# Kernel tuning notes

Hardware: AMD Instinct MI355X
Metric: run time of the kernel (lower is better)

Reference implementation:

```python
import jax, jax.numpy as jnp
import numpy as np

D = 192          # d_model = d_perc = d_tech
H = 3            # n_heads
HD = D // H      # head_dim = 64
FP = 128         # fingerprint_dim
EPS_LN = 1e-5


def _layernorm(x, g, b):
    mu = jnp.mean(x, axis=-1, keepdims=True)
    var = jnp.var(x, axis=-1, keepdims=True)
    return (x - mu) * jax.lax.rsqrt(var + EPS_LN) * g + b


def setup_inputs() -> dict:
    key = jax.random.key(0)
    ks = jax.random.split(key, 32)
    B = 65536
    s = 0.05
    inp = {
        'perc_vec': jax.random.normal(ks[0], (B, D), jnp.float32),
        'tech_vec': jax.random.normal(ks[1], (B, D), jnp.float32),
        # proj_p / proj_t (torch Linear: [out, in])
        'Wp': jax.random.normal(ks[2], (D, D), jnp.float32) * s,
        'bp': jax.random.normal(ks[3], (D,), jnp.float32) * s,
        'Wt': jax.random.normal(ks[4], (D, D), jnp.float32) * s,
        'bt': jax.random.normal(ks[5], (D,), jnp.float32) * s,
        # MultiheadAttention packed in-proj [3D, D] and out-proj [D, D]
        'in_w': jax.random.normal(ks[6], (3 * D, D), jnp.float32) * s,
        'in_b': jax.random.normal(ks[7], (3 * D,), jnp.float32) * s,
        'out_w': jax.random.normal(ks[8], (D, D), jnp.float32) * s,
        'out_b': jax.random.normal(ks[9], (D,), jnp.float32) * s,
        # FFN
        'ffn_w1': jax.random.normal(ks[10], (2 * D, D), jnp.float32) * s,
        'ffn_b1': jax.random.normal(ks[11], (2 * D,), jnp.float32) * s,
        'ffn_w2': jax.random.normal(ks[12], (D, 2 * D), jnp.float32) * s,
        'ffn_b2': jax.random.normal(ks[13], (D,), jnp.float32) * s,
        # LayerNorms
        'ln1_g': jnp.ones((D,), jnp.float32),
        'ln1_b': jnp.zeros((D,), jnp.float32),
        'ln2_g': jnp.ones((D,), jnp.float32),
        'ln2_b': jnp.zeros((D,), jnp.float32),
        # classifier head
        'cls_w1': jax.random.normal(ks[14], (D, D), jnp.float32) * s,
        'cls_b1': jax.random.normal(ks[15], (D,), jnp.float32) * s,
        'cls_w2': jax.random.normal(ks[16], (3, D), jnp.float32) * s,
        'cls_b2': jax.random.normal(ks[17], (3,), jnp.float32) * s,
        # fingerprint head
        'fp_w': jax.random.normal(ks[18], (FP, D), jnp.float32) * s,
        'fp_b': jax.random.normal(ks[19], (FP,), jnp.float32) * s,
    }
    return inp


def reference(perc_vec, tech_vec, Wp, bp, Wt, bt, in_w, in_b, out_w, out_b,
              ffn_w1, ffn_b1, ffn_w2, ffn_b2, ln1_g, ln1_b, ln2_g, ln2_b,
              cls_w1, cls_b1, cls_w2, cls_b2, fp_w, fp_b):
    B = perc_vec.shape[0]
    # projections -> 2-token sequence [B, 2, D]
    p = perc_vec @ Wp.T + bp
    t = tech_vec @ Wt.T + bt
    seq = jnp.stack([p, t], axis=1)

    # self-attention (eval mode, no dropout)
    qkv = seq @ in_w.T + in_b                     # [B, 2, 3D]
    q, k, v = jnp.split(qkv, 3, axis=-1)
    q = q.reshape(B, 2, H, HD).transpose(0, 2, 1, 3)  # [B, H, 2, HD]
    k = k.reshape(B, 2, H, HD).transpose(0, 2, 1, 3)
    v = v.reshape(B, 2, H, HD).transpose(0, 2, 1, 3)
    scores = jnp.einsum('bhqd,bhkd->bhqk', q, k) / np.sqrt(HD).astype(np.float32)
    attn = jax.nn.softmax(scores, axis=-1)
    ctx = jnp.einsum('bhqk,bhkd->bhqd', attn, v)      # [B, H, 2, HD]
    ctx = ctx.transpose(0, 2, 1, 3).reshape(B, 2, D)
    attn_out = ctx @ out_w.T + out_b

    x = _layernorm(seq + attn_out, ln1_g, ln1_b)
    h = jax.nn.relu(x @ ffn_w1.T + ffn_b1)
    ffn = h @ ffn_w2.T + ffn_b2
    x = _layernorm(x + ffn, ln2_g, ln2_b)

    z = x.mean(axis=1)                                # [B, D]
    logits = jax.nn.relu(z @ cls_w1.T + cls_b1) @ cls_w2.T + cls_b2  # [B, 3]
    probs = jax.nn.sigmoid(logits)
    fp = z @ fp_w.T + fp_b
    fp = fp / jnp.maximum(jnp.linalg.norm(fp, axis=-1, keepdims=True), 1e-12)
    # (presence_p, decode_reliability, artifact_risk, fingerprint)
    return probs[:, 0:1], probs[:, 1:2], probs[:, 2:3], fp
```

## Files before the change

kernel.cpp:

```cpp
#include <hip/hip_runtime.h>
#include <hip/hip_bf16.h>
#include <math.h>

#define D 192
#define RPB 16
typedef unsigned short u16;
typedef __attribute__((ext_vector_type(8))) short short8;
typedef __attribute__((ext_vector_type(4))) float float4v;

__device__ __forceinline__ float b2f(u16 u){ union{unsigned i; float f;}c; c.i=(unsigned)u<<16; return c.f; }
__device__ __forceinline__ u16  f2b(float f){
    union{float f; unsigned i;}c; c.f=f;
    unsigned r = c.i + 0x7FFFu + ((c.i>>16)&1u);
    return (u16)(r>>16);
}
__device__ __forceinline__ float sel4(float a0,float a1,float a2,float a3,int s){
    return s==0?a0:(s==1?a1:(s==2?a2:a3));
}

#define WP_OFF   0
#define WT_OFF   36864
#define INW_OFF  73728
#define OUTW_OFF 184320
#define FW1_OFF  221184
#define FW2_OFF  294912
#define CW1_OFF  368640
#define FPW_OFF  405504
#define W_TOTAL  430080

__global__ __launch_bounds__(256)
void cvt_weights(const float* __restrict__ Wp, const float* __restrict__ Wt,
                 const float* __restrict__ in_w, const float* __restrict__ out_w,
                 const float* __restrict__ fw1, const float* __restrict__ fw2,
                 const float* __restrict__ cw1, const float* __restrict__ fpw,
                 u16* __restrict__ ws)
{
    int idx = blockIdx.x * 256 + threadIdx.x;
    if (idx >= W_TOTAL) return;
    const float* src; int off; int K = 192;
    if      (idx < WT_OFF)   { src = Wp;   off = WP_OFF; }
    else if (idx < INW_OFF)  { src = Wt;   off = WT_OFF; }
    else if (idx < OUTW_OFF) { src = in_w; off = INW_OFF; }
    else if (idx < FW1_OFF)  { src = out_w;off = OUTW_OFF; }
    else if (idx < FW2_OFF)  { src = fw1;  off = FW1_OFF; }
    else if (idx < CW1_OFF)  { src = fw2;  off = FW2_OFF; K = 384; }
    else if (idx < FPW_OFF)  { src = cw1;  off = CW1_OFF; }
    else                     { src = fpw;  off = FPW_OFF; }
    int lin = idx - off;
    int n = lin / K, k = lin - n*K;
    int swz = ((n>>4)*(K>>5) + (k>>5))*512 + ((n&15)<<5) + (k&31);
    ws[off + swz] = f2b(src[lin]);
}

template<int KT, int MT>
__device__ __forceinline__ void load_afrags(short8 (&A)[MT][KT], const u16* base,
                                            int stride, int lane16, int quad)
{
    #pragma unroll
    for (int mt = 0; mt < MT; ++mt)
        #pragma unroll
        for (int ks = 0; ks < KT; ++ks)
            A[mt][ks] = *(const short8*)(base + (mt*16 + lane16)*stride + ks*32 + quad*8);
}

template<int KT, int MT, int NTW>
__device__ __forceinline__ void run_gemm(const short8 (&A)[MT][KT],
    const u16* __restrict__ wsb, const float* __restrict__ bias,
    u16* dst, float* dstf, int dstride,
    const u16* resid, int rstride, bool relu, int rmul, int roff,
    int wave, int lane16, int quad)
{
    #pragma unroll
    for (int i = 0; i < NTW; ++i) {
        int nt = wave + 4*i, n0 = nt*16;
        float4v c[MT];
        #pragma unroll
        for (int mt = 0; mt < MT; ++mt) c[mt] = (float4v){0.f,0.f,0.f,0.f};
        #pragma unroll
        for (int ks = 0; ks < KT; ++ks) {
            short8 b = *(const short8*)(wsb + (size_t)((nt*KT + ks)<<9) + (lane16<<5) + (quad<<3));
            #pragma unroll
            for (int mt = 0; mt < MT; ++mt)
                c[mt] = __builtin_amdgcn_mfma_f32_16x16x32_bf16(A[mt][ks], b, c[mt], 0,0,0);
        }
        float bv = bias[n0 + lane16];
        #pragma unroll
        for (int mt = 0; mt < MT; ++mt)
            #pragma unroll
            for (int ii = 0; ii < 4; ++ii) {
                int dr = (mt*16 + quad*4 + ii)*rmul + roff;
                float v = c[mt][ii] + bv;
                if (resid) v += b2f(resid[dr*rstride + n0 + lane16]);
                if (relu)  v = fmaxf(v, 0.f);
                if (dst) dst [dr*dstride + n0 + lane16] = f2b(v);
                else     dstf[dr*dstride + n0 + lane16] = v;
            }
    }
}

#define S1 200
#define SH 392
#define A_STG_P 0
#define A_STG_T 3200
#define A_SEQ 12544
#define A_CTX 0
#define A_X1  12544
#define A_H   0
#define A_Z   0
#define A_CH  3200
#define A_FPF 6400
#define ARENA_U16 18944

__global__ __launch_bounds__(256, 3)
void fusion_mfma_kernel(
    const float* __restrict__ perc, const float* __restrict__ tech,
    const float* __restrict__ bp,   const float* __restrict__ bt,
    const float* __restrict__ in_b, const float* __restrict__ out_b,
    const float* __restrict__ fb1,  const float* __restrict__ fb2,
    const float* __restrict__ ln1g, const float* __restrict__ ln1b,
    const float* __restrict__ ln2g, const float* __restrict__ ln2b,
    const float* __restrict__ cb1,  const float* __restrict__ cw2,
    const float* __restrict__ cb2,  const float* __restrict__ fpb,
    const u16*   __restrict__ ws,
    float* __restrict__ out, int B)
{
    __shared__ __align__(16) u16 arena[ARENA_U16];
    __shared__ __align__(16) float satt[16][3][4];
    __shared__ float wavered[4][32][2];
    __shared__ float srn[16];

    const int tid = threadIdx.x;
    const int wave = tid >> 6, lane = tid & 63;
    const int lane16 = lane & 15, quad = lane >> 4;
    const int row0 = blockIdx.x * RPB;
    float* fpf = (float*)(arena + A_FPF);

    #pragma unroll
    for (int it = 0; it < 3; ++it) {
        int idx = it*256 + tid;
        int arr = idx >= 384 ? 1 : 0;
        int rem = arr ? idx - 384 : idx;
        int r = rem / 24, g = rem - r*24;
        const float* src = arr ? tech : perc;
        const float4* s4 = (const float4*)(src + (size_t)(row0 + r)*D + g*8);
        float4 lo = s4[0], hi = s4[1];
        short8 o;
        o[0]=(short)f2b(lo.x); o[1]=(short)f2b(lo.y); o[2]=(short)f2b(lo.z); o[3]=(short)f2b(lo.w);
        o[4]=(short)f2b(hi.x); o[5]=(short)f2b(hi.y); o[6]=(short)f2b(hi.z); o[7]=(short)f2b(hi.w);
        *(short8*)(arena + (arr ? A_STG_T : A_STG_P) + r*S1 + g*8) = o;
    }
    __syncthreads();

    {
        short8 A1[1][6];
        load_afrags<6,1>(A1, arena + A_STG_P, S1, lane16, quad);
        run_gemm<6,1,3>(A1, ws + WP_OFF, bp, arena + A_SEQ, nullptr, S1,
                        nullptr, 0, false, 2, 0, wave, lane16, quad);
        load_afrags<6,1>(A1, arena + A_STG_T, S1, lane16, quad);
        run_gemm<6,1,3>(A1, ws + WT_OFF, bt, arena + A_SEQ, nullptr, S1,
                        nullptr, 0, false, 2, 1, wave, lane16, quad);
    }
    __syncthreads();

    short8 A2[2][6];
    load_afrags<6,2>(A2, arena + A_SEQ, S1, lane16, quad);
    {
        float* satt_w = (float*)arena;
        #pragma unroll
        for (int i = 0; i < 3; ++i) {
            int nt = wave + 4*i;
            float4v ck[2] = {(float4v){0,0,0,0},(float4v){0,0,0,0}};
            #pragma unroll
            for (int ks = 0; ks < 6; ++ks) {
                short8 b = *(const short8*)(ws + INW_OFF + 192*192 + ((nt*6+ks)<<9) + (lane16<<5) + (quad<<3));
                ck[0] = __builtin_amdgcn_mfma_f32_16x16x32_bf16(A2[0][ks], b, ck[0], 0,0,0);
                ck[1] = __builtin_amdgcn_mfma_f32_16x16x32_bf16(A2[1][ks], b, ck[1], 0,0,0);
            }
            float bvk = in_b[192 + nt*16 + lane16];
            float4v cq[2] = {(float4v){0,0,0,0},(float4v){0,0,0,0}};
            #pragma unroll
            for (int ks = 0; ks < 6; ++ks) {
                short8 b = *(const short8*)(ws + INW_OFF + ((nt*6+ks)<<9) + (lane16<<5) + (quad<<3));
                cq[0] = __builtin_amdgcn_mfma_f32_16x16x32_bf16(A2[0][ks], b, cq[0], 0,0,0);
                cq[1] = __builtin_amdgcn_mfma_f32_16x16x32_bf16(A2[1][ks], b, cq[1], 0,0,0);
            }
            float bvq = in_b[nt*16 + lane16];
            #pragma unroll
            for (int mt = 0; mt < 2; ++mt)
                #pragma unroll
                for (int p = 0; p < 2; ++p) {
                    float q0 = cq[mt][2*p] + bvq, q1 = cq[mt][2*p+1] + bvq;
                    float k0 = ck[mt][2*p] + bvk, k1 = ck[mt][2*p+1] + bvk;
                    float vv0 = q0*k0, vv1 = q0*k1, vv2 = q1*k0, vv3 = q1*k1;
                    vv0 += __shfl_xor(vv0, 1); vv0 += __shfl_xor(vv0, 2);
                    vv0 += __shfl_xor(vv0, 4); vv0 += __shfl_xor(vv0, 8);
                    vv1 += __shfl_xor(vv1, 1); vv1 += __shfl_xor(vv1, 2);
                    vv1 += __shfl_xor(vv1, 4); vv1 += __shfl_xor(vv1, 8);
                    vv2 += __shfl_xor(vv2, 1); vv2 += __shfl_xor(vv2, 2);
                    vv2 += __shfl_xor(vv2, 4); vv2 += __shfl_xor(vv2, 8);
                    vv3 += __shfl_xor(vv3, 1); vv3 += __shfl_xor(vv3, 2);
                    vv3 += __shfl_xor(vv3, 4); vv3 += __shfl_xor(vv3, 8);
                    if ((lane16 >> 2) == i) {
                        int c = lane16 & 3;
                        satt_w[(wave*16 + (2*quad + p + 8*mt))*12 + i*4 + c] =
                            sel4(vv0, vv1, vv2, vv3, c);
                    }
                }
        }
    }
    __syncthreads();

    if (tid < 96) {
        const float* satt_w = (const float*)arena;
        int r = tid / 6, rem = tid - r*6;
        int h = rem >> 1, qt = rem & 1;
        float s0 = 0.f, s1 = 0.f;
        #pragma unroll
        for (int w = 0; w < 4; ++w) {
            s0 += satt_w[(w*16 + r)*12 + h*4 + qt*2 + 0];
            s1 += satt_w[(w*16 + r)*12 + h*4 + qt*2 + 1];
        }
        s0 *= 0.125f; s1 *= 0.125f;
        float m = fmaxf(s0, s1);
        float e0 = expf(s0 - m), e1 = expf(s1 - m);
        float inv = 1.f / (e0 + e1);
        satt[r][h][qt*2 + 0] = e0 * inv;
        satt[r][h][qt*2 + 1] = e1 * inv;
    }
    __syncthreads();

    #pragma unroll
    for (int i = 0; i < 3; ++i) {
        int nt = wave + 4*i, col = nt*16 + lane16;
        float4v cv[2] = {(float4v){0,0,0,0},(float4v){0,0,0,0}};
        #pragma unroll
        for (int ks = 0; ks < 6; ++ks) {
            short8 b = *(const short8*)(ws + INW_OFF + 384*192 + ((nt*6+ks)<<9) + (lane16<<5) + (quad<<3));
            cv[0] = __builtin_amdgcn_mfma_f32_16x16x32_bf16(A2[0][ks], b, cv[0], 0,0,0);
            cv[1] = __builtin_amdgcn_mfma_f32_16x16x32_bf16(A2[1][ks], b, cv[1], 0,0,0);
        }
        float bv = in_b[384 + col];
        #pragma unroll
        for (int mt = 0; mt < 2; ++mt)
            #pragma unroll
            for (int p = 0; p < 2; ++p) {
                float v0 = cv[mt][2*p] + bv, v1 = cv[mt][2*p+1] + bv;
                int r = 2*quad + p + 8*mt;
                float4 pa = *(const float4*)&satt[r][i][0];
                arena[A_CTX + (2*r    )*S1 + col] = f2b(pa.x*v0 + pa.y*v1);
                arena[A_CTX + (2*r + 1)*S1 + col] = f2b(pa.z*v0 + pa.w*v1);
            }
    }
    __syncthreads();

    {
        short8 Ac[2][6];
        load_afrags<6,2>(Ac, arena + A_CTX, S1, lane16, quad);
        float sa[2][4], s2a[2][4];
        #pragma unroll
        for (int mt = 0; mt < 2; ++mt)
            #pragma unroll
            for (int ii = 0; ii < 4; ++ii) { sa[mt][ii] = 0.f; s2a[mt][ii] = 0.f; }
        #pragma unroll
        for (int i = 0; i < 3; ++i) {
            int nt = wave + 4*i, col = nt*16 + lane16;
            float4v c[2] = {(float4v){0,0,0,0},(float4v){0,0,0,0}};
            #pragma unroll
            for (int ks = 0; ks < 6; ++ks) {
                short8 b = *(const short8*)(ws + OUTW_OFF + ((nt*6+ks)<<9) + (lane16<<5) + (quad<<3));
                c[0] = __builtin_amdgcn_mfma_f32_16x16x32_bf16(Ac[0][ks], b, c[0], 0,0,0);
                c[1] = __builtin_amdgcn_mfma_f32_16x16x32_bf16(Ac[1][ks], b, c[1], 0,0,0);
            }
            float bv = out_b[col];
            #pragma unroll
            for (int mt = 0; mt < 2; ++mt)
                #pragma unroll
                for (int ii = 0; ii < 4; ++ii) {
                    int row = quad*4 + ii + 16*mt;
                    float v = c[mt][ii] + bv + b2f(arena[A_SEQ + row*S1 + col]);
                    arena[A_X1 + row*S1 + col] = f2b(v);
                    sa[mt][ii] += v; s2a[mt][ii] += v*v;
                }
        }
        #pragma unroll
        for (int mt = 0; mt < 2; ++mt)
            #pragma unroll
            for (int ii = 0; ii < 4; ++ii) {
                float s = sa[mt][ii], s2 = s2a[mt][ii];
                s  += __shfl_xor(s, 1);  s  += __shfl_xor(s, 2);
                s  += __shfl_xor(s, 4);  s  += __shfl_xor(s, 8);
                s2 += __shfl_xor(s2, 1); s2 += __shfl_xor(s2, 2);
                s2 += __shfl_xor(s2, 4); s2 += __shfl_xor(s2, 8);
                sa[mt][ii] = s; s2a[mt][ii] = s2;
            }
        int l = lane16;
        float rowlo = sel4(sa[0][0], sa[0][1], sa[0][2], sa[0][3], l & 3);
        float rowhi = sel4(sa[1][0], sa[1][1], sa[1][2], sa[1][3], l & 3);
        float row2lo = sel4(s2a[0][0], s2a[0][1], s2a[0][2], s2a[0][3], l & 3);
        float row2hi = sel4(s2a[1][0], s2a[1][1], s2a[1][2], s2a[1][3], l & 3);
        float sv = (l & 4) ? rowhi : rowlo;
        float s2v = (l & 4) ? row2hi : row2lo;
        float val = (l & 8) ? s2v : sv;
        wavered[wave][quad*4 + (l & 3) + 16*((l >> 2) & 1)][l >> 3] = val;
    }
    __syncthreads();

    #pragma unroll
    for (int it = 0; it < 3; ++it) {
        int idx = it*256 + tid;
        int tok = idx / 24, g = idx - tok*24;
        float s  = wavered[0][tok][0] + wavered[1][tok][0] + wavered[2][tok][0] + wavered[3][tok][0];
        float s2 = wavered[0][tok][1] + wavered[1][tok][1] + wavered[2][tok][1] + wavered[3][tok][1];
        float mu = s * (1.f/192.f);
        float rs = rsqrtf(s2 * (1.f/192.f) - mu*mu + 1e-5f);
        float4 ga = ((const float4*)(ln1g + g*8))[0], gb = ((const float4*)(ln1g + g*8))[1];
        float4 ba = ((const float4*)(ln1b + g*8))[0], bb = ((const float4*)(ln1b + g*8))[1];
        float gg[8]  = {ga.x,ga.y,ga.z,ga.w,gb.x,gb.y,gb.z,gb.w};
        float bbv[8] = {ba.x,ba.y,ba.z,ba.w,bb.x,bb.y,bb.z,bb.w};
        u16* p = arena + A_X1 + tok*S1 + g*8;
        short8 v = *(const short8*)p;
        short8 o;
        #pragma unroll
        for (int j = 0; j < 8; ++j)
            o[j] = (short)f2b((b2f((u16)v[j]) - mu)*rs*gg[j] + bbv[j]);
        *(short8*)p = o;
    }
    __syncthreads();

    {
        short8 Ax[2][6];
        load_afrags<6,2>(Ax, arena + A_X1, S1, lane16, quad);
        run_gemm<6,2,6>(Ax, ws + FW1_OFF, fb1, arena + A_H, nullptr, SH,
                        nullptr, 0, true, 1, 0, wave, lane16, quad);
    }
    __syncthreads();

    {
        float4v c2[3][2];
        #pragma unroll
        for (int i = 0; i < 3; ++i) { c2[i][0] = (float4v){0,0,0,0}; c2[i][1] = (float4v){0,0,0,0}; }
        #pragma unroll
        for (int kc = 0; kc < 2; ++kc) {
            short8 Af[2][6];
            load_afrags<6,2>(Af, arena + A_H + kc*192, SH, lane16, quad);
            #pragma unroll
            for (int i = 0; i < 3; ++i) {
                int nt = wave + 4*i;
                #pragma unroll
                for (int ks = 0; ks < 6; ++ks) {
                    short8 b = *(const short8*)(ws + FW2_OFF + ((nt*12 + kc*6 + ks)<<9) + (lane16<<5) + (quad<<3));
                    c2[i][0] = __builtin_amdgcn_mfma_f32_16x16x32_bf16(Af[0][ks], b, c2[i][0], 0,0,0);
                    c2[i][1] = __builtin_amdgcn_mfma_f32_16x16x32_bf16(Af[1][ks], b, c2[i][1], 0,0,0);
                }
            }
        }
        #pragma unroll
        for (int i = 0; i < 3; ++i) {
            int col = (wave + 4*i)*16 + lane16;
            float bv = fb2[col];
            #pragma unroll
            for (int mt = 0; mt < 2; ++mt)
                #pragma unroll
                for (int ii = 0; ii < 4; ++ii) {
                    int row = quad*4 + ii + 16*mt;
                    c2[i][mt][ii] += bv + b2f(arena[A_X1 + row*S1 + col]);
                }
        }
        float sa[2][4], s2a[2][4];
        #pragma unroll
        for (int mt = 0; mt < 2; ++mt)
            #pragma unroll
            for (int ii = 0; ii < 4; ++ii) {
                float a0 = c2[0][mt][ii], a1 = c2[1][mt][ii], a2 = c2[2][mt][ii];
                float s = a0 + a1 + a2;
                float s2 = a0*a0 + a1*a1 + a2*a2;
                s  += __shfl_xor(s, 1);  s  += __shfl_xor(s, 2);
                s  += __shfl_xor(s, 4);  s  += __shfl_xor(s, 8);
                s2 += __shfl_xor(s2, 1); s2 += __shfl_xor(s2, 2);
                s2 += __shfl_xor(s2, 4); s2 += __shfl_xor(s2, 8);
                sa[mt][ii] = s; s2a[mt][ii] = s2;
            }
        int l = lane16;
        float rowlo = sel4(sa[0][0], sa[0][1], sa[0][2], sa[0][3], l & 3);
        float rowhi = sel4(sa[1][0], sa[1][1], sa[1][2], sa[1][3], l & 3);
        float row2lo = sel4(s2a[0][0], s2a[0][1], s2a[0][2], s2a[0][3], l & 3);
        float row2hi = sel4(s2a[1][0], s2a[1][1], s2a[1][2], s2a[1][3], l & 3);
        float sv = (l & 4) ? rowhi : rowlo;
        float s2v = (l & 4) ? row2hi : row2lo;
        float val = (l & 8) ? s2v : sv;
        wavered[wave][quad*4 + (l & 3) + 16*((l >> 2) & 1)][l >> 3] = val;
        __syncthreads();
        float mus[2][2][2], rss[2][2][2];
        #pragma unroll
        for (int mt = 0; mt < 2; ++mt)
            #pragma unroll
            for (int p = 0; p < 2; ++p) {
                int r = 2*quad + p + 8*mt;
                #pragma unroll
                for (int tk = 0; tk < 2; ++tk) {
                    int row = 2*r + tk;
                    float s  = wavered[0][row][0] + wavered[1][row][0] + wavered[2][row][0] + wavered[3][row][0];
                    float s2 = wavered[0][row][1] + wavered[1][row][1] + wavered[2][row][1] + wavered[3][row][1];
                    float mu = s * (1.f/192.f);
                    mus[mt][p][tk] = mu;
                    rss[mt][p][tk] = rsqrtf(s2 * (1.f/192.f) - mu*mu + 1e-5f);
                }
            }
        #pragma unroll
        for (int i = 0; i < 3; ++i) {
            int col = (wave + 4*i)*16 + lane16;
            float g = ln2g[col], bb = ln2b[col];
            #pragma unroll
            for (int mt = 0; mt < 2; ++mt)
                #pragma unroll
                for (int p = 0; p < 2; ++p) {
                    int r = 2*quad + p + 8*mt;
                    float n0v = (c2[i][mt][2*p]   - mus[mt][p][0]) * rss[mt][p][0] * g + bb;
                    float n1v = (c2[i][mt][2*p+1] - mus[mt][p][1]) * rss[mt][p][1] * g + bb;
                    arena[A_Z + r*S1 + col] = f2b(0.5f*(n0v + n1v));
                }
        }
    }
    __syncthreads();

    {
        short8 A1[1][6];
        load_afrags<6,1>(A1, arena + A_Z, S1, lane16, quad);
        run_gemm<6,1,3>(A1, ws + CW1_OFF, cb1, arena + A_CH, nullptr, S1,
                        nullptr, 0, true, 1, 0, wave, lane16, quad);
        run_gemm<6,1,2>(A1, ws + FPW_OFF, fpb, nullptr, fpf, 128,
                        nullptr, 0, false, 1, 0, wave, lane16, quad);
    }
    __syncthreads();

    if (tid < 192) {
        int g4 = tid >> 2, sub = tid & 3;
        int r = g4 / 3, cc = g4 - r*3;
        const float* w = cw2 + (size_t)cc * D + sub*48;
        const u16* hr = arena + A_CH + r*S1 + sub*48;
        float a = 0.f;
        #pragma unroll
        for (int i = 0; i < 6; ++i) {
            short8 hv = *(const short8*)(hr + i*8);
            float4 w0 = ((const float4*)w)[2*i], w1 = ((const float4*)w)[2*i+1];
            float wv[8] = {w0.x,w0.y,w0.z,w0.w,w1.x,w1.y,w1.z,w1.w};
            #pragma unroll
            for (int j = 0; j < 8; ++j) a += wv[j] * b2f((u16)hv[j]);
        }
        a += __shfl_xor(a, 1); a += __shfl_xor(a, 2);
        if (sub == 0) {
            a += cb2[cc];
            out[(size_t)cc * B + (size_t)(row0 + r)] = 1.f / (1.f + expf(-a));
        }
    } else {
        int t = tid - 192;
        int r = t >> 2, sub = t & 3;
        const float4* fp4 = (const float4*)(fpf + r*128 + sub*32);
        float s2 = 0.f;
        #pragma unroll
        for (int i = 0; i < 8; ++i) {
            float4 v = fp4[i];
            s2 += v.x*v.x + v.y*v.y + v.z*v.z + v.w*v.w;
        }
        s2 += __shfl_xor(s2, 1); s2 += __shfl_xor(s2, 2);
        if (sub == 0) srn[r] = 1.f / fmaxf(sqrtf(s2), 1e-12f);
    }
    __syncthreads();

    #pragma unroll
    for (int it = 0; it < 2; ++it) {
        int idx = it*256 + tid;
        int r = idx >> 5, c = idx & 31;
        float4 v = ((const float4*)(fpf + r*128))[c];
        float sc = srn[r];
        float4 o; o.x = v.x*sc; o.y = v.y*sc; o.z = v.z*sc; o.w = v.w*sc;
        ((float4*)(out + (size_t)3*B + (size_t)(row0 + r)*128))[c] = o;
    }
}

extern "C" void kernel_launch(void* const* d_in, const int* in_sizes, int n_in,
                              void* d_out, int out_size, void* d_ws, size_t ws_size,
                              hipStream_t stream) {
    if (ws_size < (size_t)W_TOTAL * 2) return;

    const float* perc = (const float*)d_in[0];
    const float* tech = (const float*)d_in[1];
    const float* Wp   = (const float*)d_in[2];
    const float* bp   = (const float*)d_in[3];
    const float* Wt   = (const float*)d_in[4];
    const float* bt   = (const float*)d_in[5];
    const float* in_w = (const float*)d_in[6];
    const float* in_b = (const float*)d_in[7];
    const float* ow   = (const float*)d_in[8];
    const float* ob   = (const float*)d_in[9];
    const float* fw1  = (const float*)d_in[10];
    const float* fb1  = (const float*)d_in[11];
    const float* fw2  = (const float*)d_in[12];
    const float* fb2  = (const float*)d_in[13];
    const float* ln1g = (const float*)d_in[14];
    const float* ln1b = (const float*)d_in[15];
    const float* ln2g = (const float*)d_in[16];
    const float* ln2b = (const float*)d_in[17];
    const float* cw1  = (const float*)d_in[18];
    const float* cb1  = (const float*)d_in[19];
    const float* cw2  = (const float*)d_in[20];
    const float* cb2  = (const float*)d_in[21];
    const float* fpw  = (const float*)d_in[22];
    const float* fpb  = (const float*)d_in[23];

    u16* ws = (u16*)d_ws;
    int B = in_sizes[0] / D;

    hipLaunchKernelGGL(cvt_weights, dim3((W_TOTAL + 255)/256), dim3(256), 0, stream,
                       Wp, Wt, in_w, ow, fw1, fw2, cw1, fpw, ws);

    hipLaunchKernelGGL(fusion_mfma_kernel, dim3(B / RPB), dim3(256), 0, stream,
                       perc, tech, bp, bt, in_b, ob, fb1, fb2,
                       ln1g, ln1b, ln2g, ln2b, cb1, cw2, cb2, fpb,
                       ws, (float*)d_out, B);
}
```

Before: 419.6 us.

## Split A-fragment loads per row tile to cut VGPRs and raise occupancy

Restructures each MFMA GEMM stage (QKV, V, out-proj, FFN1, FFN2) to hold A fragments for one 16-row tile at a time instead of both, and raises launch bounds from 3 to 4 blocks per SIMD. The intent is lower register pressure so more waves are resident, hiding latency. In exchange, B weight fragments are now loaded from global/L2 twice (once per row tile) and there is less MFMA independence within each chain. The attention V stage no longer reuses the QKV-stage A fragments and reloads them from LDS.

```diff
diff --git a/kernel.cpp b/kernel.cpp
--- a/kernel.cpp
+++ b/kernel.cpp
@@ -111,7 +111,7 @@
 #define A_FPF 6400
 #define ARENA_U16 18944
 
-__global__ __launch_bounds__(256, 3)
+__global__ __launch_bounds__(256, 4)
 void fusion_mfma_kernel(
     const float* __restrict__ perc, const float* __restrict__ tech,
     const float* __restrict__ bp,   const float* __restrict__ bt,
@@ -162,35 +162,35 @@
     }
     __syncthreads();
 
-    short8 A2[2][6];
-    load_afrags<6,2>(A2, arena + A_SEQ, S1, lane16, quad);
     {
         float* satt_w = (float*)arena;
         #pragma unroll
-        for (int i = 0; i < 3; ++i) {
-            int nt = wave + 4*i;
-            float4v ck[2] = {(float4v){0,0,0,0},(float4v){0,0,0,0}};
-            #pragma unroll
-            for (int ks = 0; ks < 6; ++ks) {
-                short8 b = *(const short8*)(ws + INW_OFF + 192*192 + ((nt*6+ks)<<9) + (lane16<<5) + (quad<<3));
-                ck[0] = __builtin_amdgcn_mfma_f32_16x16x32_bf16(A2[0][ks], b, ck[0], 0,0,0);
-                ck[1] = __builtin_amdgcn_mfma_f32_16x16x32_bf16(A2[1][ks], b, ck[1], 0,0,0);
-            }
-            float bvk = in_b[192 + nt*16 + lane16];
-            float4v cq[2] = {(float4v){0,0,0,0},(float4v){0,0,0,0}};
-            #pragma unroll
-            for (int ks = 0; ks < 6; ++ks) {
-                short8 b = *(const short8*)(ws + INW_OFF + ((nt*6+ks)<<9) + (lane16<<5) + (quad<<3));
-                cq[0] = __builtin_amdgcn_mfma_f32_16x16x32_bf16(A2[0][ks], b, cq[0], 0,0,0);
-                cq[1] = __builtin_amdgcn_mfma_f32_16x16x32_bf16(A2[1][ks], b, cq[1], 0,0,0);
-            }
-            float bvq = in_b[nt*16 + lane16];
-            #pragma unroll
-            for (int mt = 0; mt < 2; ++mt)
+        for (int mt = 0; mt < 2; ++mt) {
+            short8 Ah[6];
+            #pragma unroll
+            for (int ks = 0; ks < 6; ++ks)
+                Ah[ks] = *(const short8*)(arena + A_SEQ + (mt*16 + lane16)*S1 + ks*32 + quad*8);
+            #pragma unroll
+            for (int i = 0; i < 3; ++i) {
+                int nt = wave + 4*i;
+                float4v ck = (float4v){0,0,0,0};
+                #pragma unroll
+                for (int ks = 0; ks < 6; ++ks) {
+                    short8 b = *(const short8*)(ws + INW_OFF + 192*192 + ((nt*6+ks)<<9) + (lane16<<5) + (quad<<3));
+                    ck = __builtin_amdgcn_mfma_f32_16x16x32_bf16(Ah[ks], b, ck, 0,0,0);
+                }
+                float bvk = in_b[192 + nt*16 + lane16];
+                float4v cq = (float4v){0,0,0,0};
+                #pragma unroll
+                for (int ks = 0; ks < 6; ++ks) {
+                    short8 b = *(const short8*)(ws + INW_OFF + ((nt*6+ks)<<9) + (lane16<<5) + (quad<<3));
+                    cq = __builtin_amdgcn_mfma_f32_16x16x32_bf16(Ah[ks], b, cq, 0,0,0);
+                }
+                float bvq = in_b[nt*16 + lane16];
                 #pragma unroll
                 for (int p = 0; p < 2; ++p) {
-                    float q0 = cq[mt][2*p] + bvq, q1 = cq[mt][2*p+1] + bvq;
-                    float k0 = ck[mt][2*p] + bvk, k1 = ck[mt][2*p+1] + bvk;
+                    float q0 = cq[2*p] + bvq, q1 = cq[2*p+1] + bvq;
+                    float k0 = ck[2*p] + bvk, k1 = ck[2*p+1] + bvk;
                     float vv0 = q0*k0, vv1 = q0*k1, vv2 = q1*k0, vv3 = q1*k1;
                     vv0 += __shfl_xor(vv0, 1); vv0 += __shfl_xor(vv0, 2);
                     vv0 += __shfl_xor(vv0, 4); vv0 += __shfl_xor(vv0, 8);
@@ -206,6 +206,7 @@
                             sel4(vv0, vv1, vv2, vv3, c);
                     }
                 }
+            }
         }
     }
     __syncthreads();
@@ -230,57 +231,61 @@
     __syncthreads();
 
     #pragma unroll
-    for (int i = 0; i < 3; ++i) {
-        int nt = wave + 4*i, col = nt*16 + lane16;
-        float4v cv[2] = {(float4v){0,0,0,0},(float4v){0,0,0,0}};
-        #pragma unroll
-        for (int ks = 0; ks < 6; ++ks) {
-            short8 b = *(const short8*)(ws + INW_OFF + 384*192 + ((nt*6+ks)<<9) + (lane16<<5) + (quad<<3));
-            cv[0] = __builtin_amdgcn_mfma_f32_16x16x32_bf16(A2[0][ks], b, cv[0], 0,0,0);
-            cv[1] = __builtin_amdgcn_mfma_f32_16x16x32_bf16(A2[1][ks], b, cv[1], 0,0,0);
-        }
-        float bv = in_b[384 + col];
-        #pragma unroll
-        for (int mt = 0; mt < 2; ++mt)
+    for (int mt = 0; mt < 2; ++mt) {
+        short8 Ah[6];
+        #pragma unroll
+        for (int ks = 0; ks < 6; ++ks)
+            Ah[ks] = *(const short8*)(arena + A_SEQ + (mt*16 + lane16)*S1 + ks*32 + quad*8);
+        #pragma unroll
+        for (int i = 0; i < 3; ++i) {
+            int nt = wave + 4*i, col = nt*16 + lane16;
+            float4v cv = (float4v){0,0,0,0};
+            #pragma unroll
+            for (int ks = 0; ks < 6; ++ks) {
+                short8 b = *(const short8*)(ws + INW_OFF + 384*192 + ((nt*6+ks)<<9) + (lane16<<5) + (quad<<3));
+                cv = __builtin_amdgcn_mfma_f32_16x16x32_bf16(Ah[ks], b, cv, 0,0,0);
+            }
+            float bv = in_b[384 + col];
             #pragma unroll
             for (int p = 0; p < 2; ++p) {
-                float v0 = cv[mt][2*p] + bv, v1 = cv[mt][2*p+1] + bv;
+                float v0 = cv[2*p] + bv, v1 = cv[2*p+1] + bv;
                 int r = 2*quad + p + 8*mt;
                 float4 pa = *(const float4*)&satt[r][i][0];
                 arena[A_CTX + (2*r    )*S1 + col] = f2b(pa.x*v0 + pa.y*v1);
                 arena[A_CTX + (2*r + 1)*S1 + col] = f2b(pa.z*v0 + pa.w*v1);
             }
+        }
     }
     __syncthreads();
 
     {
-        short8 Ac[2][6];
-        load_afrags<6,2>(Ac, arena + A_CTX, S1, lane16, quad);
         float sa[2][4], s2a[2][4];
         #pragma unroll
-        for (int mt = 0; mt < 2; ++mt)
+        for (int mt = 0; mt < 2; ++mt) {
+            short8 Ah[6];
+            #pragma unroll
+            for (int ks = 0; ks < 6; ++ks)
+                Ah[ks] = *(const short8*)(arena + A_CTX + (mt*16 + lane16)*S1 + ks*32 + quad*8);
             #pragma unroll
             for (int ii = 0; ii < 4; ++ii) { sa[mt][ii] = 0.f; s2a[mt][ii] = 0.f; }
-        #pragma unroll
-        for (int i = 0; i < 3; ++i) {
-            int nt = wave + 4*i, col = nt*16 + lane16;
-            float4v c[2] = {(float4v){0,0,0,0},(float4v){0,0,0,0}};
-            #pragma unroll
-            for (int ks = 0; ks < 6; ++ks) {
-                short8 b = *(const short8*)(ws + OUTW_OFF + ((nt*6+ks)<<9) + (lane16<<5) + (quad<<3));
-                c[0] = __builtin_amdgcn_mfma_f32_16x16x32_bf16(Ac[0][ks], b, c[0], 0,0,0);
-                c[1] = __builtin_amdgcn_mfma_f32_16x16x32_bf16(Ac[1][ks], b, c[1], 0,0,0);
-            }
-            float bv = out_b[col];
-            #pragma unroll
-            for (int mt = 0; mt < 2; ++mt)
+            #pragma unroll
+            for (int i = 0; i < 3; ++i) {
+                int nt = wave + 4*i, col = nt*16 + lane16;
+                float4v c = (float4v){0,0,0,0};
+                #pragma unroll
+                for (int ks = 0; ks < 6; ++ks) {
+                    short8 b = *(const short8*)(ws + OUTW_OFF + ((nt*6+ks)<<9) + (lane16<<5) + (quad<<3));
+                    c = __builtin_amdgcn_mfma_f32_16x16x32_bf16(Ah[ks], b, c, 0,0,0);
+                }
+                float bv = out_b[col];
                 #pragma unroll
                 for (int ii = 0; ii < 4; ++ii) {
                     int row = quad*4 + ii + 16*mt;
-                    float v = c[mt][ii] + bv + b2f(arena[A_SEQ + row*S1 + col]);
+                    float v = c[ii] + bv + b2f(arena[A_SEQ + row*S1 + col]);
                     arena[A_X1 + row*S1 + col] = f2b(v);
                     sa[mt][ii] += v; s2a[mt][ii] += v*v;
                 }
+            }
         }
         #pragma unroll
         for (int mt = 0; mt < 2; ++mt)
@@ -328,9 +333,12 @@
     __syncthreads();
 
     {
-        short8 Ax[2][6];
-        load_afrags<6,2>(Ax, arena + A_X1, S1, lane16, quad);
-        run_gemm<6,2,6>(Ax, ws + FW1_OFF, fb1, arena + A_H, nullptr, SH,
+        short8 Ax[1][6];
+        load_afrags<6,1>(Ax, arena + A_X1, S1, lane16, quad);
+        run_gemm<6,1,6>(Ax, ws + FW1_OFF, fb1, arena + A_H, nullptr, SH,
+                        nullptr, 0, true, 1, 0, wave, lane16, quad);
+        load_afrags<6,1>(Ax, arena + A_X1 + 16*S1, S1, lane16, quad);
+        run_gemm<6,1,6>(Ax, ws + FW1_OFF, fb1, arena + A_H + 16*SH, nullptr, SH,
                         nullptr, 0, true, 1, 0, wave, lane16, quad);
     }
     __syncthreads();
@@ -340,20 +348,23 @@
         #pragma unroll
         for (int i = 0; i < 3; ++i) { c2[i][0] = (float4v){0,0,0,0}; c2[i][1] = (float4v){0,0,0,0}; }
         #pragma unroll
-        for (int kc = 0; kc < 2; ++kc) {
-            short8 Af[2][6];
-            load_afrags<6,2>(Af, arena + A_H + kc*192, SH, lane16, quad);
-            #pragma unroll
-            for (int i = 0; i < 3; ++i) {
-                int nt = wave + 4*i;
-                #pragma unroll
-                for (int ks = 0; ks < 6; ++ks) {
-                    short8 b = *(const short8*)(ws + FW2_OFF + ((nt*12 + kc*6 + ks)<<9) + (lane16<<5) + (quad<<3));
-                    c2[i][0] = __builtin_amdgcn_mfma_f32_16x16x32_bf16(Af[0][ks], b, c2[i][0], 0,0,0);
-                    c2[i][1] = __builtin_amdgcn_mfma_f32_16x16x32_bf16(Af[1][ks], b, c2[i][1], 0,0,0);
-                }
-            }
-        }
+        for (int kc = 0; kc < 2; ++kc)
+            #pragma unroll
+            for (int mt = 0; mt < 2; ++mt) {
+                short8 Ah[6];
+                #pragma unroll
+                for (int ks = 0; ks < 6; ++ks)
+                    Ah[ks] = *(const short8*)(arena + A_H + (mt*16 + lane16)*SH + kc*192 + ks*32 + quad*8);
+                #pragma unroll
+                for (int i = 0; i < 3; ++i) {
+                    int nt = wave + 4*i;
+                    #pragma unroll
+                    for (int ks = 0; ks < 6; ++ks) {
+                        short8 b = *(const short8*)(ws + FW2_OFF + ((nt*12 + kc*6 + ks)<<9) + (lane16<<5) + (quad<<3));
+                        c2[i][mt] = __builtin_amdgcn_mfma_f32_16x16x32_bf16(Ah[ks], b, c2[i][mt], 0,0,0);
+                    }
+                }
+            }
         #pragma unroll
         for (int i = 0; i < 3; ++i) {
             int col = (wave + 4*i)*16 + lane16;
```

After: 524.0 us. 1.25x slower.
